# Kernel tuning notes

Hardware: AMD Instinct MI355X
Metric: run time of the kernel (lower is better)

Reference implementation:

```python
import jax, jax.numpy as jnp
import numpy as np

V = 50257   # vocab_size
BLOCK = 1024
D = 768     # n_embd
H = 12      # n_head
L = 2       # n_layer
B = 4
T = 1024
EPS = 1e-5


def _ln(x, g, b):
    mu = jnp.mean(x, axis=-1, keepdims=True)
    var = jnp.var(x, axis=-1, keepdims=True)
    return (x - mu) * jax.lax.rsqrt(var + EPS) * g + b


def setup_inputs() -> dict:
    key = jax.random.key(0)
    ks = jax.random.split(key, 10)
    def n(k, shape, std=0.02):
        return jax.random.normal(k, shape, jnp.float32) * std
    proj_std = (2 * L) ** -0.5  # set_scale init in the torch code
    return dict(
        idx=jax.random.randint(ks[0], (B, T), 0, V),
        layer_num=0,
        wte=n(ks[1], (V, D)),
        wpe=n(ks[2], (BLOCK, D)),
        ln1_g=jnp.ones((L, D)), ln1_b=jnp.zeros((L, D)),
        attn_w=n(ks[3], (L, D, 3 * D)), attn_b=jnp.zeros((L, 3 * D)),
        proj_w=n(ks[4], (L, D, D), proj_std), proj_b=jnp.zeros((L, D)),
        ln2_g=jnp.ones((L, D)), ln2_b=jnp.zeros((L, D)),
        fc_w=n(ks[5], (L, D, 4 * D)), fc_b=jnp.zeros((L, 4 * D)),
        fc2_w=n(ks[6], (L, 4 * D, D), proj_std), fc2_b=jnp.zeros((L, D)),
        lnf_g=jnp.ones((D,)), lnf_b=jnp.zeros((D,)),
        lm_w=n(ks[7], (D, V)),
    )


def _gpt(idx, wte, wpe, ln1_g, ln1_b, attn_w, attn_b, proj_w, proj_b,
         ln2_g, ln2_b, fc_w, fc_b, fc2_w, fc2_b, lnf_g, lnf_b, lm_w):
    b, t = idx.shape
    hd = D // H
    x = wte[idx] + wpe[:t]                      # [B,T,D]
    causal = jnp.tril(jnp.ones((t, t), bool))   # [T,T]
    for l in range(L):
        h = _ln(x, ln1_g[l], ln1_b[l])
        qkv = h @ attn_w[l] + attn_b[l]          # [B,T,3D]
        q, k, v = jnp.split(qkv, 3, axis=-1)
        q = q.reshape(b, t, H, hd)
        k = k.reshape(b, t, H, hd)
        v = v.reshape(b, t, H, hd)
        att = jnp.einsum('bqhd,bkhd->bhqk', q, k) * (1.0 / np.sqrt(hd))
        att = jnp.where(causal, att, -jnp.inf)
        att = jax.nn.softmax(att, axis=-1)
        y = jnp.einsum('bhqk,bkhd->bqhd', att, v).reshape(b, t, D)
        x = x + (y @ proj_w[l] + proj_b[l])
        h2 = _ln(x, ln2_g[l], ln2_b[l])
        h2 = jax.nn.gelu(h2 @ fc_w[l] + fc_b[l], approximate=True)  # tanh GELU
        x = x + (h2 @ fc2_w[l] + fc2_b[l])
    x = _ln(x, lnf_g, lnf_b)
    return x @ lm_w                             # [B,T,V] logits


def reference(idx, layer_num, wte, wpe, ln1_g, ln1_b, attn_w, attn_b,
              proj_w, proj_b, ln2_g, ln2_b, fc_w, fc_b, fc2_w, fc2_b,
              lnf_g, lnf_b, lm_w):
    # layer_num is unused in the forward math (pipeline-stage bookkeeping)
    return _gpt(idx, wte, wpe, ln1_g, ln1_b, attn_w, attn_b, proj_w, proj_b,
                ln2_g, ln2_b, fc_w, fc_b, fc2_w, fc2_b, lnf_g, lnf_b, lm_w)
```

## Files before the change

### kernel.cpp

```cpp
#include <hip/hip_runtime.h>
#include <hip/hip_bf16.h>
#include <cstdint>
#include <cstddef>

typedef __bf16 bf16_t;
typedef __bf16 bf16x8 __attribute__((ext_vector_type(8)));
typedef float f32x4 __attribute__((ext_vector_type(4)));

#define GLB_AS(p) ((__attribute__((address_space(1))) void*)(void*)(p))
#define LDS_AS(p) ((__attribute__((address_space(3))) void*)(p))

__device__ __forceinline__ float wave_red_sum(float v) {
#pragma unroll
  for (int o = 1; o < 64; o <<= 1) v += __shfl_xor(v, o, 64);
  return v;
}

__device__ __forceinline__ float gelu_tanh(float v) {
  float c = 0.7978845608028654f * (v + 0.044715f * v * v * v);
  return 0.5f * v * (1.0f + tanhf(c));
}

__device__ __forceinline__ f32x4 mfma16(f32x4 a, f32x4 b, f32x4 c) {
  return __builtin_amdgcn_mfma_f32_16x16x32_bf16(
      __builtin_bit_cast(bf16x8, a), __builtin_bit_cast(bf16x8, b), c, 0, 0, 0);
}

__device__ __forceinline__ int swz(int off) { return off ^ ((off >> 3) & 0x70); }
__device__ __forceinline__ int swz64(int off) { return off ^ ((off >> 3) & 0x30); }

#define PHASE_WAIT()                                    \
  asm volatile("s_waitcnt lgkmcnt(0)" ::: "memory");    \
  __builtin_amdgcn_sched_barrier(0)

__global__ __launch_bounds__(256) void embed_ln_k(const int* __restrict__ idx,
                                                  const float* __restrict__ wte,
                                                  const float* __restrict__ wpe,
                                                  const float* __restrict__ g,
                                                  const float* __restrict__ b,
                                                  float* __restrict__ x,
                                                  bf16_t* __restrict__ out) {
  const int m = blockIdx.x;
  const int tid = threadIdx.x;
  const int tok = idx[m];
  const int t = m & 1023;
  float v[3];
#pragma unroll
  for (int i = 0; i < 3; ++i) {
    const int d = tid + i * 256;
    v[i] = wte[(size_t)tok * 768 + d] + wpe[(size_t)t * 768 + d];
    x[(size_t)m * 768 + d] = v[i];
  }
  float s = v[0] + v[1] + v[2];
  float q = v[0] * v[0] + v[1] * v[1] + v[2] * v[2];
  s = wave_red_sum(s);
  q = wave_red_sum(q);
  __shared__ float sm[8];
  const int wave = tid >> 6, lane = tid & 63;
  if (lane == 0) { sm[wave] = s; sm[4 + wave] = q; }
  __syncthreads();
  s = sm[0] + sm[1] + sm[2] + sm[3];
  q = sm[4] + sm[5] + sm[6] + sm[7];
  const float mu = s * (1.0f / 768.0f);
  const float var = q * (1.0f / 768.0f) - mu * mu;
  const float rs = rsqrtf(var + 1e-5f);
  bf16_t* orow = out + (size_t)m * 768;
#pragma unroll
  for (int i = 0; i < 3; ++i) {
    const int d = tid + i * 256;
    orow[d] = (bf16_t)((v[i] - mu) * rs * g[d] + b[d]);
  }
}

__global__ __launch_bounds__(256) void ln_k(const float* __restrict__ x,
                                            const float* __restrict__ g,
                                            const float* __restrict__ b,
                                            bf16_t* __restrict__ out) {
  const int row = blockIdx.x;
  const int tid = threadIdx.x;
  const float* xr = x + (size_t)row * 768;
  float v0 = xr[tid], v1 = xr[tid + 256], v2 = xr[tid + 512];
  float s = v0 + v1 + v2;
  float q = v0 * v0 + v1 * v1 + v2 * v2;
  s = wave_red_sum(s);
  q = wave_red_sum(q);
  __shared__ float sm[8];
  const int wave = tid >> 6, lane = tid & 63;
  if (lane == 0) { sm[wave] = s; sm[4 + wave] = q; }
  __syncthreads();
  s = sm[0] + sm[1] + sm[2] + sm[3];
  q = sm[4] + sm[5] + sm[6] + sm[7];
  const float mu = s * (1.0f / 768.0f);
  const float var = q * (1.0f / 768.0f) - mu * mu;
  const float rs = rsqrtf(var + 1e-5f);
  bf16_t* orow = out + (size_t)row * 768;
#pragma unroll
  for (int i = 0; i < 3; ++i) {
    const int d = tid + i * 256;
    const float v = (i == 0 ? v0 : (i == 1 ? v1 : v2));
    orow[d] = (bf16_t)((v - mu) * rs * g[d] + b[d]);
  }
}

struct TJob { const float* W; bf16_t* WT; int K, N, Npad, blk0, nbx; };
struct TJobs { TJob j[9]; };

__global__ __launch_bounds__(256) void transp_all(TJobs jobs) {
  __shared__ float tile[32][33];
  const int bidx = blockIdx.x;
  int ji = 0;
#pragma unroll
  for (int u = 1; u < 9; ++u)
    if (bidx >= jobs.j[u].blk0) ji = u;
  const TJob jb = jobs.j[ji];
  const int lb = bidx - jb.blk0;
  const int n0 = (lb % jb.nbx) * 32, k0 = (lb / jb.nbx) * 32;
  const int tx = threadIdx.x, ty = threadIdx.y;
#pragma unroll
  for (int i = 0; i < 4; ++i) {
    const int k = k0 + ty + i * 8, n = n0 + tx;
    tile[ty + i * 8][tx] = (k < jb.K && n < jb.N) ? jb.W[(size_t)k * jb.N + n] : 0.0f;
  }
  __syncthreads();
#pragma unroll
  for (int i = 0; i < 4; ++i) {
    const int n = n0 + ty + i * 8, k = k0 + tx;
    if (n < jb.Npad && k < jb.K) jb.WT[(size_t)n * jb.K + k] = (bf16_t)tile[tx][ty + i * 8];
  }
}

__global__ __launch_bounds__(256) void vtr_k(const bf16_t* __restrict__ qkv,
                                             bf16_t* __restrict__ vt) {
  __shared__ bf16_t tile[64][72];
  const int bh = blockIdx.y;
  const int h = bh % 12, b = bh / 12;
  const int t0 = blockIdx.x * 64;
  const int tx = threadIdx.x & 63;
  const int wv = threadIdx.x >> 6;
#pragma unroll
  for (int i = 0; i < 16; ++i) {
    const int r = wv * 16 + i;
    tile[r][tx] = qkv[(size_t)(b * 1024 + t0 + r) * 2304 + 1536 + h * 64 + tx];
  }
  __syncthreads();
#pragma unroll
  for (int i = 0; i < 16; ++i) {
    const int d = wv * 16 + i;
    vt[((size_t)bh * 64 + d) * 1024 + t0 + tx] = tile[tx][d];
  }
}

template <int EPI>
__global__ __launch_bounds__(512, 2) void gemm256p(const bf16_t* __restrict__ A,
                                                   const bf16_t* __restrict__ BT,
                                                   const float* __restrict__ bias,
                                                   void* __restrict__ outp,
                                                   int M, int N, int K, int Nout,
                                                   int ntiles) {
  __shared__ __align__(16) char lds[131072];
  const int tid = threadIdx.x;
  const int lane = tid & 63, wave = tid >> 6;
  const int wr = wave >> 2, wc = wave & 3;
  const int fr = lane & 15, fq = lane >> 4;

  const int nmblk = M >> 8;
  const int G = gridDim.x;
  const int flat = blockIdx.x;
  const int xcd = flat & 7, rest = flat >> 3;
  const int q8 = G >> 3, r8 = G & 7;
  const int bid = (xcd < r8 ? xcd * (q8 + 1) : r8 * (q8 + 1) + (xcd - r8) * q8) + rest;
  const int qt = ntiles / G, rt = ntiles % G;
  const int tstart = bid * qt + (bid < rt ? bid : rt);
  const int cnt = qt + (bid < rt ? 1 : 0);
  if (cnt == 0) return;
  const int NT = K >> 6;
  const int sEnd = (tstart + cnt) * NT;

  int srow[4], scb[4];
#pragma unroll
  for (int u = 0; u < 4; ++u) {
    const int s = swz(u * 8192 + tid * 16);
    srow[u] = s >> 7;
    scb[u] = s & 127;
  }
  const char* Abase = (const char*)A;
  const char* Bbase = (const char*)BT;

  auto stageA = [&](int pi, int u, int m0x, int tauK) {
    const char* src = Abase + ((size_t)(m0x + srow[u]) * K + tauK * 64) * 2 + scb[u];
    __builtin_amdgcn_global_load_lds(GLB_AS(src),
        LDS_AS(&lds[pi * 32768 + u * 8192 + wave * 1024]), 16, 0, 0);
  };
  auto stageB = [&](int pi, int u, int n0x, int tauK) {
    const char* src = Bbase + ((size_t)(n0x + srow[u]) * K + tauK * 64) * 2 + scb[u];
    __builtin_amdgcn_global_load_lds(GLB_AS(src),
        LDS_AS(&lds[65536 + pi * 32768 + u * 8192 + wave * 1024]), 16, 0, 0);
  };
  auto rdA = [&](int pi, int msub, int i, int kk) -> f32x4 {
    const int row = wr * 128 + msub * 64 + i * 16 + fr;
    const int off = swz(row * 128 + kk * 64 + fq * 16);
    return *(const f32x4*)(&lds[pi * 32768 + off]);
  };
  auto rdB = [&](int pi, int j, int kk) -> f32x4 {
    const int row = wc * 64 + j * 16 + fr;
    const int off = swz(row * 128 + kk * 64 + fq * 16);
    return *(const f32x4*)(&lds[65536 + pi * 32768 + off]);
  };

  int m0 = (tstart % nmblk) << 8, n0 = (tstart / nmblk) << 8;
  int m1 = m0, n1 = n0, t1 = 1;
  int m2 = m0, n2 = n0, t2 = 2;
  auto adv = [&](int& mx, int& nx, int& tx) {
    if (++tx == NT) { tx = 0; mx += 256; if (mx >= M) { mx = 0; nx += 256; } }
  };

  f32x4 acc[8][4] = {};
  f32x4 a_[4][2], b_[4][2];

  stageA(0, 0, m0, 0); stageA(0, 1, m0, 0); stageA(0, 2, m0, 0); stageA(0, 3, m0, 0);
  stageB(0, 0, n0, 0); stageB(0, 1, n0, 0); stageB(0, 2, n0, 0); stageB(0, 3, n0, 0);
  stageA(1, 0, m1, t1); stageA(1, 2, m1, t1); stageB(1, 0, n1, t1); stageB(1, 1, n1, t1);
  stageA(1, 1, m1, t1); stageA(1, 3, m1, t1);
  asm volatile("s_waitcnt vmcnt(6)" ::: "memory");
  __builtin_amdgcn_s_barrier();

  int pi = 0;
  int s = tstart * NT;
  for (int t = 0; t < cnt; ++t) {
    for (int tau = 0; tau < NT; ++tau, ++s) {
      const bool h1 = (s + 1 < sEnd), h2 = (s + 2 < sEnd);
#pragma unroll
      for (int i = 0; i < 4; ++i) { a_[i][0] = rdA(pi, 0, i, 0); a_[i][1] = rdA(pi, 0, i, 1); }
#pragma unroll
      for (int j = 0; j < 2; ++j) { b_[j][0] = rdB(pi, j, 0); b_[j][1] = rdB(pi, j, 1); }
      if (h1) { stageB(pi ^ 1, 2, n1, t1); stageB(pi ^ 1, 3, n1, t1); }
      __builtin_amdgcn_s_barrier();
      PHASE_WAIT();
      __builtin_amdgcn_s_setprio(1);
#pragma unroll
      for (int i = 0; i < 4; ++i)
#pragma unroll
        for (int j = 0; j < 2; ++j) {
          acc[i][j] = mfma16(a_[i][0], b_[j][0], acc[i][j]);
          acc[i][j] = mfma16(a_[i][1], b_[j][1], acc[i][j]);
        }
      __builtin_amdgcn_s_setprio(0);
      __builtin_amdgcn_s_barrier();
#pragma unroll
      for (int j = 0; j < 2; ++j) { b_[2 + j][0] = rdB(pi, 2 + j, 0); b_[2 + j][1] = rdB(pi, 2 + j, 1); }
      if (h2) { stageA(pi, 0, m2, t2); stageA(pi, 2, m2, t2); }
      __builtin_amdgcn_s_barrier();
      PHASE_WAIT();
      __builtin_amdgcn_s_setprio(1);
#pragma unroll
      for (int i = 0; i < 4; ++i)
#pragma unroll
        for (int j = 0; j < 2; ++j) {
          acc[i][2 + j] = mfma16(a_[i][0], b_[2 + j][0], acc[i][2 + j]);
          acc[i][2 + j] = mfma16(a_[i][1], b_[2 + j][1], acc[i][2 + j]);
        }
      __builtin_amdgcn_s_setprio(0);
      __builtin_amdgcn_s_barrier();
#pragma unroll
      for (int i = 0; i < 4; ++i) { a_[i][0] = rdA(pi, 1, i, 0); a_[i][1] = rdA(pi, 1, i, 1); }
      if (h2) { stageB(pi, 0, n2, t2); stageB(pi, 1, n2, t2); }
      __builtin_amdgcn_s_barrier();
      PHASE_WAIT();
      __builtin_amdgcn_s_setprio(1);
#pragma unroll
      for (int i = 0; i < 4; ++i)
#pragma unroll
        for (int j = 0; j < 2; ++j) {
          acc[4 + i][j] = mfma16(a_[i][0], b_[j][0], acc[4 + i][j]);
          acc[4 + i][j] = mfma16(a_[i][1], b_[j][1], acc[4 + i][j]);
        }
      __builtin_amdgcn_s_setprio(0);
      __builtin_amdgcn_s_barrier();
      if (h2) {
        stageA(pi, 1, m2, t2); stageA(pi, 3, m2, t2);
        asm volatile("s_waitcnt vmcnt(6)" ::: "memory");
      } else {
        asm volatile("s_waitcnt vmcnt(0)" ::: "memory");
      }
      __builtin_amdgcn_s_barrier();
      __builtin_amdgcn_sched_barrier(0);
      __builtin_amdgcn_s_setprio(1);
#pragma unroll
      for (int i = 0; i < 4; ++i)
#pragma unroll
        for (int j = 0; j < 2; ++j) {
          acc[4 + i][2 + j] = mfma16(a_[i][0], b_[2 + j][0], acc[4 + i][2 + j]);
          acc[4 + i][2 + j] = mfma16(a_[i][1], b_[2 + j][1], acc[4 + i][2 + j]);
        }
      __builtin_amdgcn_s_setprio(0);
      __builtin_amdgcn_s_barrier();
      pi ^= 1;
      adv(m1, n1, t1);
      adv(m2, n2, t2);
    }

#pragma unroll
    for (int i8 = 0; i8 < 8; ++i8) {
#pragma unroll
      for (int j4 = 0; j4 < 4; ++j4) {
        const int r0 = m0 + wr * 128 + i8 * 16 + fq * 4;
        const int c = n0 + wc * 64 + j4 * 16 + fr;
        float bv = 0.0f;
        if constexpr (EPI != 3) bv = bias[c];
#pragma unroll
        for (int e = 0; e < 4; ++e) {
          const int r = r0 + e;
          float v = acc[i8][j4][e] + bv;
          if constexpr (EPI == 0) {
            ((bf16_t*)outp)[(size_t)r * N + c] = (bf16_t)v;
          } else if constexpr (EPI == 1) {
            ((bf16_t*)outp)[(size_t)r * N + c] = (bf16_t)gelu_tanh(v);
          } else {
            if (c < Nout) ((float*)outp)[(size_t)r * Nout + c] = v;
          }
        }
      }
    }
#pragma unroll
    for (int i8 = 0; i8 < 8; ++i8)
#pragma unroll
      for (int j4 = 0; j4 < 4; ++j4) acc[i8][j4] = (f32x4){0.0f, 0.0f, 0.0f, 0.0f};
    m0 += 256; if (m0 >= M) { m0 = 0; n0 += 256; }
  }
}

__global__ __launch_bounds__(256) void gemm128p(const bf16_t* __restrict__ A,
                                                const bf16_t* __restrict__ BT,
                                                const float* __restrict__ bias,
                                                float* __restrict__ resid,
                                                int M, int N, int K) {
  __shared__ __align__(16) char lds[32768];
  const int tid = threadIdx.x;
  const int lane = tid & 63, wave = tid >> 6;
  const int wr = wave >> 1, wc = wave & 1;
  const int fr = lane & 15, fq = lane >> 4;

  const int nmblk = M >> 7;
  const int nwg = gridDim.x;
  const int flat = blockIdx.x;
  const int xcd = flat & 7, rest = flat >> 3;
  const int q8 = nwg >> 3, r8 = nwg & 7;
  const int wgid = (xcd < r8 ? xcd * (q8 + 1) : r8 * (q8 + 1) + (xcd - r8) * q8) + rest;
  const int m0 = (wgid % nmblk) * 128;
  const int n0 = (wgid / nmblk) * 128;
  const int NT = K >> 5;

  int srow[2], scb[2];
#pragma unroll
  for (int u = 0; u < 2; ++u) {
    const int s = swz64(u * 4096 + tid * 16);
    srow[u] = s >> 6;
    scb[u] = s & 63;
  }
  const char* Abase = (const char*)A;
  const char* Bbase = (const char*)BT;

  auto stage = [&](int pi, int tauK) {
#pragma unroll
    for (int u = 0; u < 2; ++u) {
      const char* srcA = Abase + ((size_t)(m0 + srow[u]) * K + tauK * 32) * 2 + scb[u];
      __builtin_amdgcn_global_load_lds(GLB_AS(srcA),
          LDS_AS(&lds[pi * 8192 + u * 4096 + wave * 1024]), 16, 0, 0);
      const char* srcB = Bbase + ((size_t)(n0 + srow[u]) * K + tauK * 32) * 2 + scb[u];
      __builtin_amdgcn_global_load_lds(GLB_AS(srcB),
          LDS_AS(&lds[16384 + pi * 8192 + u * 4096 + wave * 1024]), 16, 0, 0);
    }
  };
  auto rdA = [&](int pi, int i) -> f32x4 {
    const int off = swz64((wr * 64 + i * 16 + fr) * 64 + fq * 16);
    return *(const f32x4*)(&lds[pi * 8192 + off]);
  };
  auto rdB = [&](int pi, int j) -> f32x4 {
    const int off = swz64((wc * 64 + j * 16 + fr) * 64 + fq * 16);
    return *(const f32x4*)(&lds[16384 + pi * 8192 + off]);
  };

  f32x4 acc[4][4] = {};

  stage(0, 0); stage(1, 1);
  asm volatile("s_waitcnt vmcnt(4)" ::: "memory");
  __builtin_amdgcn_s_barrier();

  for (int s = 0; s < NT; ++s) {
    const int pi = s & 1;
    f32x4 a_[4], b_[4];
#pragma unroll
    for (int i = 0; i < 4; ++i) a_[i] = rdA(pi, i);
#pragma unroll
    for (int j = 0; j < 4; ++j) b_[j] = rdB(pi, j);
    PHASE_WAIT();
    __builtin_amdgcn_s_setprio(1);
#pragma unroll
    for (int i = 0; i < 4; ++i)
#pragma unroll
      for (int j = 0; j < 4; ++j) acc[i][j] = mfma16(a_[i], b_[j], acc[i][j]);
    __builtin_amdgcn_s_setprio(0);
    __builtin_amdgcn_s_barrier();
    if (s + 2 < NT) {
      stage(pi, s + 2);
      asm volatile("s_waitcnt vmcnt(4)" ::: "memory");
    } else {
      asm volatile("s_waitcnt vmcnt(0)" ::: "memory");
    }
    __builtin_amdgcn_s_barrier();
  }

#pragma unroll
  for (int i = 0; i < 4; ++i) {
#pragma unroll
    for (int j = 0; j < 4; ++j) {
      const int r0 = m0 + wr * 64 + i * 16 + fq * 4;
      const int c = n0 + wc * 64 + j * 16 + fr;
      const float bv = bias[c];
#pragma unroll
      for (int e = 0; e < 4; ++e) {
        const int r = r0 + e;
        resid[(size_t)r * N + c] += acc[i][j][e] + bv;
      }
    }
  }
}

__global__ __launch_bounds__(256) void fattn_k(const bf16_t* __restrict__ qkv,
                                               const bf16_t* __restrict__ vt,
                                               bf16_t* __restrict__ y) {
  __shared__ bf16_t Pl[4][16][40];
  const int wave = threadIdx.x >> 6, lane = threadIdx.x & 63;
  const int wid = blockIdx.x * 4 + wave;
  const int qt = wid & 63;
  const int bh = wid >> 6;
  const int h = bh % 12, b = bh / 12;
  const int fr = lane & 15, fq = lane >> 4;

  const bf16_t* qrow = qkv + (size_t)(b * 1024 + qt * 16 + fr) * 2304 + h * 64;
  const bf16x8 qf0 = *(const bf16x8*)(qrow + fq * 8);
  const bf16x8 qf1 = *(const bf16x8*)(qrow + 32 + fq * 8);

  const bf16_t* kbase = qkv + (size_t)b * 1024 * 2304 + 768 + h * 64 + fq * 8;
  const bf16_t* vbase = vt + ((size_t)bh * 64 + fr) * 1024 + fq * 8;

  f32x4 o[4] = {};
  float mrun[4], lrun[4];
#pragma unroll
  for (int e = 0; e < 4; ++e) { mrun[e] = -1e30f; lrun[e] = 0.0f; }

  const int qg = qt * 16 + fq * 4;
  const int kv_end = qt * 16 + 16;

  for (int kv0 = 0; kv0 < kv_end; kv0 += 32) {
    f32x4 s0 = {}, s1 = {};
    {
      const bf16_t* k0p = kbase + (size_t)(kv0 + fr) * 2304;
      const bf16_t* k1p = kbase + (size_t)(kv0 + 16 + fr) * 2304;
      const bf16x8 kf00 = *(const bf16x8*)(k0p);
      const bf16x8 kf01 = *(const bf16x8*)(k0p + 32);
      const bf16x8 kf10 = *(const bf16x8*)(k1p);
      const bf16x8 kf11 = *(const bf16x8*)(k1p + 32);
      s0 = __builtin_amdgcn_mfma_f32_16x16x32_bf16(qf0, kf00, s0, 0, 0, 0);
      s0 = __builtin_amdgcn_mfma_f32_16x16x32_bf16(qf1, kf01, s0, 0, 0, 0);
      s1 = __builtin_amdgcn_mfma_f32_16x16x32_bf16(qf0, kf10, s1, 0, 0, 0);
      s1 = __builtin_amdgcn_mfma_f32_16x16x32_bf16(qf1, kf11, s1, 0, 0, 0);
    }
    float v0[4], v1[4];
#pragma unroll
    for (int e = 0; e < 4; ++e) {
      v0[e] = (kv0 + fr <= qg + e) ? s0[e] * 0.125f : -1e30f;
      v1[e] = (kv0 + 16 + fr <= qg + e) ? s1[e] * 0.125f : -1e30f;
    }
    float p0[4], p1[4];
#pragma unroll
    for (int e = 0; e < 4; ++e) {
      float mx = fmaxf(v0[e], v1[e]);
      mx = fmaxf(mx, __shfl_xor(mx, 1, 64));
      mx = fmaxf(mx, __shfl_xor(mx, 2, 64));
      mx = fmaxf(mx, __shfl_xor(mx, 4, 64));
      mx = fmaxf(mx, __shfl_xor(mx, 8, 64));
      const float mnew = fmaxf(mrun[e], mx);
      p0[e] = __expf(v0[e] - mnew);
      p1[e] = __expf(v1[e] - mnew);
      float rs = p0[e] + p1[e];
      rs += __shfl_xor(rs, 1, 64);
      rs += __shfl_xor(rs, 2, 64);
      rs += __shfl_xor(rs, 4, 64);
      rs += __shfl_xor(rs, 8, 64);
      const float alpha = __expf(mrun[e] - mnew);
      lrun[e] = lrun[e] * alpha + rs;
      mrun[e] = mnew;
#pragma unroll
      for (int db = 0; db < 4; ++db) o[db][e] *= alpha;
    }
#pragma unroll
    for (int e = 0; e < 4; ++e) {
      Pl[wave][fq * 4 + e][fr] = (bf16_t)p0[e];
      Pl[wave][fq * 4 + e][16 + fr] = (bf16_t)p1[e];
    }
    asm volatile("s_waitcnt lgkmcnt(0)" ::: "memory");
    const bf16x8 pf = *(const bf16x8*)(&Pl[wave][fr][fq * 8]);
#pragma unroll
    for (int db = 0; db < 4; ++db) {
      const bf16x8 vf = *(const bf16x8*)(vbase + (size_t)db * 16 * 1024 + kv0);
      o[db] = __builtin_amdgcn_mfma_f32_16x16x32_bf16(pf, vf, o[db], 0, 0, 0);
    }
  }

#pragma unroll
  for (int db = 0; db < 4; ++db) {
#pragma unroll
    for (int e = 0; e < 4; ++e) {
      const int q = qt * 16 + fq * 4 + e;
      const int d = db * 16 + fr;
      y[(size_t)(b * 1024 + q) * 768 + h * 64 + d] = (bf16_t)(o[db][e] / lrun[e]);
    }
  }
}

extern "C" void kernel_launch(void* const* d_in, const int* in_sizes, int n_in,
                              void* d_out, int out_size, void* d_ws, size_t ws_size,
                              hipStream_t stream) {
  constexpr int Bb = 4, T = 1024, Lg = 2, Vr = 50257, Vp = 50432;
  constexpr int M = Bb * T;

  const int* idx = (const int*)d_in[0];
  const float* wte = (const float*)d_in[2];
  const float* wpe = (const float*)d_in[3];
  const float* ln1_g = (const float*)d_in[4];
  const float* ln1_b = (const float*)d_in[5];
  const float* attn_w = (const float*)d_in[6];
  const float* attn_b = (const float*)d_in[7];
  const float* proj_w = (const float*)d_in[8];
  const float* proj_b = (const float*)d_in[9];
  const float* ln2_g = (const float*)d_in[10];
  const float* ln2_b = (const float*)d_in[11];
  const float* fc_w = (const float*)d_in[12];
  const float* fc_b = (const float*)d_in[13];
  const float* fc2_w = (const float*)d_in[14];
  const float* fc2_b = (const float*)d_in[15];
  const float* lnf_g = (const float*)d_in[16];
  const float* lnf_b = (const float*)d_in[17];
  const float* lm_w = (const float*)d_in[18];
  float* out = (float*)d_out;

  char* wp = (char*)d_ws;
  auto take = [&](size_t n) { char* p = wp; wp += (n + 255) & ~(size_t)255; return p; };
  bf16_t* WqkvT = (bf16_t*)take((size_t)Lg * 2304 * 768 * 2);
  bf16_t* WprojT = (bf16_t*)take((size_t)Lg * 768 * 768 * 2);
  bf16_t* WfcT = (bf16_t*)take((size_t)Lg * 3072 * 768 * 2);
  bf16_t* Wfc2T = (bf16_t*)take((size_t)Lg * 768 * 3072 * 2);
  bf16_t* WlmT = (bf16_t*)take((size_t)Vp * 768 * 2);
  float* xb = (float*)take((size_t)M * 768 * 4);
  bf16_t* hb = (bf16_t*)take((size_t)M * 768 * 2);
  bf16_t* qkvb = (bf16_t*)take((size_t)M * 2304 * 2);
  bf16_t* yb = (bf16_t*)take((size_t)M * 768 * 2);
  bf16_t* actb = (bf16_t*)take((size_t)M * 3072 * 2);
  bf16_t* vtb = (bf16_t*)take((size_t)M * 768 * 2);

  TJobs jobs;
  int blk = 0, ji = 0;
  auto addjob = [&](const float* W, bf16_t* WT, int K, int N, int Npad) {
    const int nbx = Npad / 32, nby = K / 32;
    jobs.j[ji++] = TJob{W, WT, K, N, Npad, blk, nbx};
    blk += nbx * nby;
  };
  for (int l = 0; l < Lg; ++l) {
    addjob(attn_w + (size_t)l * 768 * 2304, WqkvT + (size_t)l * 2304 * 768, 768, 2304, 2304);
    addjob(proj_w + (size_t)l * 768 * 768, WprojT + (size_t)l * 768 * 768, 768, 768, 768);
    addjob(fc_w + (size_t)l * 768 * 3072, WfcT + (size_t)l * 3072 * 768, 768, 3072, 3072);
    addjob(fc2_w + (size_t)l * 3072 * 768, Wfc2T + (size_t)l * 768 * 3072, 3072, 768, 768);
  }
  addjob(lm_w, WlmT, 768, Vr, Vp);
  transp_all<<<blk, dim3(32, 8), 0, stream>>>(jobs);

  embed_ln_k<<<M, 256, 0, stream>>>(idx, wte, wpe, ln1_g, ln1_b, xb, hb);

  for (int l = 0; l < Lg; ++l) {
    if (l > 0) ln_k<<<M, 256, 0, stream>>>(xb, ln1_g + l * 768, ln1_b + l * 768, hb);
    gemm256p<0><<<(M / 256) * (2304 / 256), 512, 0, stream>>>(
        hb, WqkvT + (size_t)l * 2304 * 768, attn_b + l * 2304, qkvb,
        M, 2304, 768, 2304, (M / 256) * (2304 / 256));
    vtr_k<<<dim3(T / 64, Bb * 12), 256, 0, stream>>>(qkvb, vtb);
    fattn_k<<<(Bb * 12 * 64) / 4, 256, 0, stream>>>(qkvb, vtb, yb);
    gemm128p<<<(M / 128) * (768 / 128), 256, 0, stream>>>(
        yb, WprojT + (size_t)l * 768 * 768, proj_b + l * 768, xb, M, 768, 768);
    ln_k<<<M, 256, 0, stream>>>(xb, ln2_g + l * 768, ln2_b + l * 768, hb);
    gemm256p<1><<<(M / 256) * (3072 / 256), 512, 0, stream>>>(
        hb, WfcT + (size_t)l * 3072 * 768, fc_b + l * 3072, actb,
        M, 3072, 768, 3072, (M / 256) * (3072 / 256));
    gemm128p<<<(M / 128) * (768 / 128), 256, 0, stream>>>(
        actb, Wfc2T + (size_t)l * 768 * 3072, fc2_b + l * 768, xb, M, 768, 3072);
  }
  ln_k<<<M, 256, 0, stream>>>(xb, lnf_g, lnf_b, hb);
  gemm256p<3><<<512, 512, 0, stream>>>(
      hb, WlmT, nullptr, out, M, Vp, 768, Vr, (M / 256) * (Vp / 256));
}
```

Measured before the change: 1.140 ms.

## Restructure GEMM main loop to load full tile fragments upfront with fewer barriers

Rewrites the persistent GEMM inner loop so that each k-step issues all A and B LDS fragment reads up front and uses partial lgkmcnt waits to overlap the reads with the first MFMA groups. The per-step block barriers drop from eight to two. Global-to-LDS staging of the step two ahead is now issued as one batch after the LDS reads finish, replacing the interleaved quarter-tile staging. This uses more registers for the second A fragment set, and fetches from global memory are bunched rather than spread across the step.

```diff
diff --git a/kernel.cpp b/kernel.cpp
--- a/kernel.cpp
+++ b/kernel.cpp
@@ -31,6 +31,10 @@
 
 #define PHASE_WAIT()                                    \
   asm volatile("s_waitcnt lgkmcnt(0)" ::: "memory");    \
+  __builtin_amdgcn_sched_barrier(0)
+
+#define LGKM_WAIT(N)                                          \
+  asm volatile("s_waitcnt lgkmcnt(" #N ")" ::: "memory");     \
   __builtin_amdgcn_sched_barrier(0)
 
 __global__ __launch_bounds__(256) void embed_ln_k(const int* __restrict__ idx,
@@ -208,95 +212,94 @@
   };
 
   int m0 = (tstart % nmblk) << 8, n0 = (tstart / nmblk) << 8;
-  int m1 = m0, n1 = n0, t1 = 1;
-  int m2 = m0, n2 = n0, t2 = 2;
   auto adv = [&](int& mx, int& nx, int& tx) {
     if (++tx == NT) { tx = 0; mx += 256; if (mx >= M) { mx = 0; nx += 256; } }
   };
 
   f32x4 acc[8][4] = {};
-  f32x4 a_[4][2], b_[4][2];
-
-  stageA(0, 0, m0, 0); stageA(0, 1, m0, 0); stageA(0, 2, m0, 0); stageA(0, 3, m0, 0);
-  stageB(0, 0, n0, 0); stageB(0, 1, n0, 0); stageB(0, 2, n0, 0); stageB(0, 3, n0, 0);
-  stageA(1, 0, m1, t1); stageA(1, 2, m1, t1); stageB(1, 0, n1, t1); stageB(1, 1, n1, t1);
-  stageA(1, 1, m1, t1); stageA(1, 3, m1, t1);
-  asm volatile("s_waitcnt vmcnt(6)" ::: "memory");
+  f32x4 a0_[4][2], a1_[4][2], b_[4][2];
+
+  int m2 = m0, n2 = n0, t2 = 0;
+  {
+#pragma unroll
+    for (int u = 0; u < 4; ++u) stageA(0, u, m2, t2);
+#pragma unroll
+    for (int u = 0; u < 4; ++u) stageB(0, u, n2, t2);
+    adv(m2, n2, t2);
+#pragma unroll
+    for (int u = 0; u < 4; ++u) stageA(1, u, m2, t2);
+#pragma unroll
+    for (int u = 0; u < 4; ++u) stageB(1, u, n2, t2);
+    adv(m2, n2, t2);
+  }
+  asm volatile("s_waitcnt vmcnt(8)" ::: "memory");
   __builtin_amdgcn_s_barrier();
 
   int pi = 0;
   int s = tstart * NT;
   for (int t = 0; t < cnt; ++t) {
     for (int tau = 0; tau < NT; ++tau, ++s) {
-      const bool h1 = (s + 1 < sEnd), h2 = (s + 2 < sEnd);
-#pragma unroll
-      for (int i = 0; i < 4; ++i) { a_[i][0] = rdA(pi, 0, i, 0); a_[i][1] = rdA(pi, 0, i, 1); }
+      const bool h2 = (s + 2 < sEnd);
+#pragma unroll
+      for (int i = 0; i < 4; ++i) { a0_[i][0] = rdA(pi, 0, i, 0); a0_[i][1] = rdA(pi, 0, i, 1); }
 #pragma unroll
       for (int j = 0; j < 2; ++j) { b_[j][0] = rdB(pi, j, 0); b_[j][1] = rdB(pi, j, 1); }
-      if (h1) { stageB(pi ^ 1, 2, n1, t1); stageB(pi ^ 1, 3, n1, t1); }
-      __builtin_amdgcn_s_barrier();
-      PHASE_WAIT();
+#pragma unroll
+      for (int j = 2; j < 4; ++j) { b_[j][0] = rdB(pi, j, 0); b_[j][1] = rdB(pi, j, 1); }
+#pragma unroll
+      for (int i = 0; i < 4; ++i) { a1_[i][0] = rdA(pi, 1, i, 0); a1_[i][1] = rdA(pi, 1, i, 1); }
+      LGKM_WAIT(12);
       __builtin_amdgcn_s_setprio(1);
 #pragma unroll
       for (int i = 0; i < 4; ++i)
 #pragma unroll
         for (int j = 0; j < 2; ++j) {
-          acc[i][j] = mfma16(a_[i][0], b_[j][0], acc[i][j]);
-          acc[i][j] = mfma16(a_[i][1], b_[j][1], acc[i][j]);
+          acc[i][j] = mfma16(a0_[i][0], b_[j][0], acc[i][j]);
+          acc[i][j] = mfma16(a0_[i][1], b_[j][1], acc[i][j]);
         }
       __builtin_amdgcn_s_setprio(0);
-      __builtin_amdgcn_s_barrier();
-#pragma unroll
-      for (int j = 0; j < 2; ++j) { b_[2 + j][0] = rdB(pi, 2 + j, 0); b_[2 + j][1] = rdB(pi, 2 + j, 1); }
-      if (h2) { stageA(pi, 0, m2, t2); stageA(pi, 2, m2, t2); }
-      __builtin_amdgcn_s_barrier();
-      PHASE_WAIT();
+      LGKM_WAIT(8);
       __builtin_amdgcn_s_setprio(1);
 #pragma unroll
       for (int i = 0; i < 4; ++i)
 #pragma unroll
         for (int j = 0; j < 2; ++j) {
-          acc[i][2 + j] = mfma16(a_[i][0], b_[2 + j][0], acc[i][2 + j]);
-          acc[i][2 + j] = mfma16(a_[i][1], b_[2 + j][1], acc[i][2 + j]);
+          acc[i][2 + j] = mfma16(a0_[i][0], b_[2 + j][0], acc[i][2 + j]);
+          acc[i][2 + j] = mfma16(a0_[i][1], b_[2 + j][1], acc[i][2 + j]);
         }
       __builtin_amdgcn_s_setprio(0);
+      LGKM_WAIT(0);
       __builtin_amdgcn_s_barrier();
-#pragma unroll
-      for (int i = 0; i < 4; ++i) { a_[i][0] = rdA(pi, 1, i, 0); a_[i][1] = rdA(pi, 1, i, 1); }
-      if (h2) { stageB(pi, 0, n2, t2); stageB(pi, 1, n2, t2); }
-      __builtin_amdgcn_s_barrier();
-      PHASE_WAIT();
+      if (h2) {
+#pragma unroll
+        for (int u = 0; u < 4; ++u) stageA(pi, u, m2, t2);
+#pragma unroll
+        for (int u = 0; u < 4; ++u) stageB(pi, u, n2, t2);
+      }
       __builtin_amdgcn_s_setprio(1);
 #pragma unroll
       for (int i = 0; i < 4; ++i)
 #pragma unroll
         for (int j = 0; j < 2; ++j) {
-          acc[4 + i][j] = mfma16(a_[i][0], b_[j][0], acc[4 + i][j]);
-          acc[4 + i][j] = mfma16(a_[i][1], b_[j][1], acc[4 + i][j]);
+          acc[4 + i][j] = mfma16(a1_[i][0], b_[j][0], acc[4 + i][j]);
+          acc[4 + i][j] = mfma16(a1_[i][1], b_[j][1], acc[4 + i][j]);
+        }
+#pragma unroll
+      for (int i = 0; i < 4; ++i)
+#pragma unroll
+        for (int j = 0; j < 2; ++j) {
+          acc[4 + i][2 + j] = mfma16(a1_[i][0], b_[2 + j][0], acc[4 + i][2 + j]);
+          acc[4 + i][2 + j] = mfma16(a1_[i][1], b_[2 + j][1], acc[4 + i][2 + j]);
         }
       __builtin_amdgcn_s_setprio(0);
-      __builtin_amdgcn_s_barrier();
       if (h2) {
-        stageA(pi, 1, m2, t2); stageA(pi, 3, m2, t2);
-        asm volatile("s_waitcnt vmcnt(6)" ::: "memory");
+        asm volatile("s_waitcnt vmcnt(8)" ::: "memory");
       } else {
         asm volatile("s_waitcnt vmcnt(0)" ::: "memory");
       }
       __builtin_amdgcn_s_barrier();
-      __builtin_amdgcn_sched_barrier(0);
-      __builtin_amdgcn_s_setprio(1);
-#pragma unroll
-      for (int i = 0; i < 4; ++i)
-#pragma unroll
-        for (int j = 0; j < 2; ++j) {
-          acc[4 + i][2 + j] = mfma16(a_[i][0], b_[2 + j][0], acc[4 + i][2 + j]);
-          acc[4 + i][2 + j] = mfma16(a_[i][1], b_[2 + j][1], acc[4 + i][2 + j]);
-        }
-      __builtin_amdgcn_s_setprio(0);
-      __builtin_amdgcn_s_barrier();
       pi ^= 1;
-      adv(m1, n1, t1);
-      adv(m2, n2, t2);
+      if (h2) adv(m2, n2, t2);
     }
 
 #pragma unroll
```

After: 1.133 ms. No clear change (-0.7%).
